# Kernel optimization log

Hardware: AMD Instinct MI355X
Metric: run time of the kernel (lower is better)

The kernel has to match this reference:

```python
import jax, jax.numpy as jnp
import numpy as np

D_MODEL = 1024
NUM_HEADS = 16
SEG = 512            # segment_size
DIL = 4              # dilation_rate
HEAD_DIM = D_MODEL // NUM_HEADS


def setup_inputs() -> dict:
    key = jax.random.key(0)
    ks = jax.random.split(key, 5)
    B, S = 4, 4096
    sc = D_MODEL ** -0.5  # keep projected activations O(1) so softmax is not saturated
    def w(k):
        return jax.random.normal(k, (D_MODEL, D_MODEL), jnp.float32) * sc
    z = jnp.zeros((D_MODEL,), jnp.float32)
    return {
        "x": jax.random.normal(ks[0], (B, S, D_MODEL), jnp.float32),
        "Wq": w(ks[1]), "bq": z,
        "Wk": w(ks[2]), "bk": z,
        "Wv": w(ks[3]), "bv": z,
        "Wo": w(ks[4]), "bo": z,
    }


def reference(x, Wq, bq, Wk, bk, Wv, bv, Wo, bo):
    B, S, D = x.shape
    H, hd, seg, r = NUM_HEADS, HEAD_DIM, SEG, DIL
    scaling = hd ** -0.5

    Q = x @ Wq + bq
    K = x @ Wk + bk
    V = x @ Wv + bv

    pad = (-S) % seg
    if pad:
        Q = jnp.pad(Q, ((0, 0), (0, pad), (0, 0)))
        K = jnp.pad(K, ((0, 0), (0, pad), (0, 0)))
        V = jnp.pad(V, ((0, 0), (0, pad), (0, 0)))
    n = (S + pad) // seg          # num_segments
    sd = seg // r                 # dilated positions per segment per head

    # [B, n, sd, r, H, hd]: position within segment = t*r + offset
    def split(t):
        return t.reshape(B, n, sd, r, H, hd)

    offs = jnp.arange(H) % r      # per-head dilation offset sj = j % r
    hidx = jnp.arange(H)
    # vectorized per-head dilated gather -> [B, n, sd, H, hd]
    Qs = split(Q)[:, :, :, offs, hidx, :]
    Ks = split(K)[:, :, :, offs, hidx, :]
    Vs = split(V)[:, :, :, offs, hidx, :]

    # diagonal q.k score per dilated position, softmax over the segment's dilated positions
    scores = jnp.einsum('bnshd,bnshd->bnsh', Qs, Ks) * scaling
    probs = jax.nn.softmax(scores, axis=2)
    attn = probs[..., None] * Vs  # [B, n, sd, H, hd]

    # scatter back to each head's dilated positions; other positions stay zero
    out = jnp.zeros((B, n, sd, r, H, hd), x.dtype)
    out = out.at[:, :, :, offs, hidx, :].set(attn)
    out = out.reshape(B, n * seg, D)[:, :S]
    return out @ Wo + bo
```

## Files before the change

kernel.cpp:

```cpp
#include <hip/hip_runtime.h>
#include <hip/hip_bf16.h>

typedef unsigned short u16;
typedef unsigned int u32;
typedef __attribute__((ext_vector_type(8))) __bf16 bf16x8;
typedef __attribute__((ext_vector_type(4))) float f32x4;

#define NB 4
#define SQ 4096
#define DM 1024
#define RPC 4096
#define S4 (4 * DM)

#define VMCNT(n) asm volatile("s_waitcnt vmcnt(" #n ")" ::: "memory")
#define BARRIER() asm volatile("s_barrier" ::: "memory")

__device__ __forceinline__ u16 f2b(float f) {
  u32 u = __builtin_bit_cast(u32, f);
  u32 r = u + 0x7fffu + ((u >> 16) & 1u);
  return (u16)(r >> 16);
}
__device__ __forceinline__ u32 cvt2(float lo, float hi) {
  u16 a = __builtin_bit_cast(u16, __float2bfloat16(lo));
  u16 b = __builtin_bit_cast(u16, __float2bfloat16(hi));
  return (u32)a | ((u32)b << 16);
}
__device__ __forceinline__ float dot2(u32 q, u32 k) {
  float ql = __builtin_bit_cast(float, q << 16);
  float qh = __builtin_bit_cast(float, q & 0xffff0000u);
  float kl = __builtin_bit_cast(float, k << 16);
  float kh = __builtin_bit_cast(float, k & 0xffff0000u);
  return ql * kl + qh * kh;
}
__device__ __forceinline__ u32 mul2(u32 v, float p) {
  float lo = __builtin_bit_cast(float, v << 16) * p;
  float hi = __builtin_bit_cast(float, v & 0xffff0000u) * p;
  return (u32)f2b(lo) | ((u32)f2b(hi) << 16);
}
__device__ __forceinline__ void gll16(const void* g, void* l) {
  __builtin_amdgcn_global_load_lds(
      (const __attribute__((address_space(1))) void*)g,
      (__attribute__((address_space(3))) void*)l, 16, 0, 0);
}

__global__ __launch_bounds__(256) void pack_x(const float* __restrict__ x,
                                              u16* __restrict__ xbT) {
  const int tid = threadIdx.x;
  const int wv = tid >> 6, l = tid & 63;
  const int gr0 = blockIdx.x * 16 + wv * 4;
#pragma unroll
  for (int it = 0; it < 4; ++it) {
    const int gr = gr0 + it;
    const int c = gr >> 12, pr = gr & 4095;
    const int b = pr >> 10;
    const int srow = ((pr & 1023) << 2) + c;
    const int m0 = pr >> 8, rloc = pr & 255;
    const float* src = x + ((size_t)(b * SQ) + srow) * DM;
    u16* dimg = xbT + (size_t)((c * 16 + m0) * 16) * 16384 + rloc * 64;
    const int swzbase = ((((l & 15) >> 1) ^ (rloc & 7)) << 3) + (l & 1) * 4;
#pragma unroll
    for (int i = 0; i < 4; ++i) {
      float4 v = *reinterpret_cast<const float4*>(src + i * 256 + l * 4);
      uint2 pk;
      pk.x = cvt2(v.x, v.y);
      pk.y = cvt2(v.z, v.w);
      const int k64 = i * 4 + (l >> 4);
      *reinterpret_cast<uint2*>(dimg + (size_t)k64 * 16384 + swzbase) = pk;
    }
  }
}

__global__ __launch_bounds__(256) void trans_qkv(const float* __restrict__ Wq,
                                                 const float* __restrict__ Wk,
                                                 const float* __restrict__ Wv,
                                                 u16* __restrict__ WTp) {
  __shared__ float T[64][65];
  const int k0 = blockIdx.x * 64, j0 = blockIdx.y * 64, c = blockIdx.z;
  const int msel = j0 >> 8;
  const float* W = (msel == 0) ? Wq : ((msel == 1) ? Wk : Wv);
  const int slot = (j0 & 255) >> 6;
  const int colbase = (c + 4 * slot) * 64;
  const int tid = threadIdx.x;
  const int rr = tid >> 6, cc = tid & 63;
#pragma unroll
  for (int it = 0; it < 16; ++it) {
    const int kk = rr + it * 4;
    T[kk][cc] = W[(size_t)(k0 + kk) * 1024 + colbase + cc];
  }
  __syncthreads();
  const int k64 = k0 >> 6;
  const int u = cc >> 3, e = cc & 7;
#pragma unroll
  for (int it = 0; it < 16; ++it) {
    const int jj = rr + it * 4;
    const int j = j0 + jj;
    const int n0 = j / 192, nrow = j - n0 * 192;
    WTp[((size_t)((c * 4 + n0) * 16 + k64)) * 12288 + nrow * 64 + (((u ^ (nrow & 7))) << 3) + e] =
        f2b(T[cc][jj]);
  }
}

__global__ __launch_bounds__(256) void trans_wo(const float* __restrict__ Wo,
                                                u16* __restrict__ WoTp) {
  __shared__ float T[64][65];
  const int j0 = blockIdx.x * 64, e0 = blockIdx.y * 64, c = blockIdx.z;
  const int rowbase = c * 64 + (j0 >> 6) * 256;
  const int tid = threadIdx.x;
  const int rr = tid >> 6, cc = tid & 63;
#pragma unroll
  for (int it = 0; it < 16; ++it) {
    const int jj = rr + it * 4;
    T[jj][cc] = Wo[(size_t)(rowbase + jj) * 1024 + e0 + cc];
  }
  __syncthreads();
  const int k64 = j0 >> 6;
  const int u = cc >> 3, e = cc & 7;
#pragma unroll
  for (int it = 0; it < 16; ++it) {
    const int ee = rr + it * 4;
    const int n = e0 + ee;
    const int n0 = n >> 8, nrow = n & 255;
    WoTp[((size_t)((c * 4 + n0) * 4 + k64)) * 16384 + nrow * 64 + (((u ^ (nrow & 7))) << 3) + e] =
        f2b(T[cc][ee]);
  }
}

__global__ __launch_bounds__(256) void bias_pack(const float* __restrict__ bq,
                                                 const float* __restrict__ bk,
                                                 const float* __restrict__ bv,
                                                 float* __restrict__ biasp) {
  const int idx = blockIdx.x * 256 + threadIdx.x;
  if (idx >= 3072) return;
  const int c = idx / 768, j = idx % 768;
  const int msel = j >> 8, jj = j & 255;
  const int col = (c + 4 * (jj >> 6)) * 64 + (jj & 63);
  const float* bb = (msel == 0) ? bq : ((msel == 1) ? bk : bv);
  biasp[idx] = bb[col];
}

__global__ __launch_bounds__(512, 1) void gemm_qkv(const u16* __restrict__ xbT,
                                                   const u16* __restrict__ WTp,
                                                   const float* __restrict__ biasp,
                                                   u16* __restrict__ QKV) {
  __shared__ __align__(16) u16 As3[3 * 16384];
  __shared__ __align__(16) u16 Bs2[2 * 12288];
  const int p = blockIdx.x;
  const int L = (p & 7) * 32 + (p >> 3);
  const int c = L >> 6, rem = L & 63;
  const int m0 = rem >> 2, n0 = rem & 3;
  const int tid = threadIdx.x;
  const int lane = tid & 63, w = tid >> 6;
  const int wm = w >> 1, wn = w & 1;
  const int l15 = lane & 15, l16 = lane >> 4;

  const u16* Asrc = xbT + (size_t)((c * 16 + m0) * 16) * 16384;
  const u16* Bsrc = WTp + (size_t)((c * 4 + n0) * 16) * 12288;

  f32x4 acc[4][6];
#pragma unroll
  for (int i = 0; i < 4; ++i)
#pragma unroll
    for (int j = 0; j < 6; ++j) acc[i][j] = (f32x4){0.f, 0.f, 0.f, 0.f};

  int abase[2], bbase[2];
#pragma unroll
  for (int kk = 0; kk < 2; ++kk) {
    const int unit = kk * 4 + l16;
    abase[kk] = (wm * 64 + l15) * 64 + ((unit ^ (l15 & 7)) << 3);
    bbase[kk] = (wn * 96 + l15) * 64 + ((unit ^ (l15 & 7)) << 3);
  }

#define ISSUE_A(kt, buf)                                                   \
  {                                                                        \
    _Pragma("unroll") for (int i = 0; i < 4; ++i)                          \
        gll16(Asrc + (size_t)(kt) * 16384 + tid * 8 + i * 4096,            \
              (char*)As3 + (buf) * 32768 + tid * 16 + i * 8192);           \
  }
#define ISSUE_B(kt, buf)                                                   \
  {                                                                        \
    _Pragma("unroll") for (int i = 0; i < 3; ++i)                          \
        gll16(Bsrc + (size_t)(kt) * 12288 + tid * 8 + i * 4096,            \
              (char*)Bs2 + (buf) * 24576 + tid * 16 + i * 8192);           \
  }

  ISSUE_A(0, 0);
  ISSUE_B(0, 0);
  ISSUE_A(1, 1);
  ISSUE_B(1, 1);
  ISSUE_A(2, 2);
  VMCNT(11);
  BARRIER();

  int abuf = 0, bbuf = 0;
#pragma unroll 1
  for (int t = 0; t < 16; ++t) {
    const u16* Ab = As3 + abuf * 16384;
    const u16* Bb = Bs2 + bbuf * 12288;
#pragma unroll
    for (int kk = 0; kk < 2; ++kk) {
      bf16x8 af[4], bv[6];
#pragma unroll
      for (int mf = 0; mf < 4; ++mf)
        af[mf] = *reinterpret_cast<const bf16x8*>(Ab + abase[kk] + mf * 1024);
#pragma unroll
      for (int nf = 0; nf < 6; ++nf)
        bv[nf] = *reinterpret_cast<const bf16x8*>(Bb + bbase[kk] + nf * 1024);
      __builtin_amdgcn_s_setprio(1);
#pragma unroll
      for (int mf = 0; mf < 4; ++mf)
#pragma unroll
        for (int nf = 0; nf < 6; ++nf)
          acc[mf][nf] = __builtin_amdgcn_mfma_f32_16x16x32_bf16(af[mf], bv[nf], acc[mf][nf], 0, 0, 0);
      __builtin_amdgcn_s_setprio(0);
    }
    if (t == 15) break;
    BARRIER();
    if (t <= 12) ISSUE_A(t + 3, abuf);
    if (t <= 13) ISSUE_B(t + 2, bbuf);
    if (t <= 12) { VMCNT(7); }
    else if (t == 13) { VMCNT(3); }
    else { VMCNT(0); }
    BARRIER();
    abuf = (abuf == 2) ? 0 : abuf + 1;
    bbuf ^= 1;
  }
#undef ISSUE_A
#undef ISSUE_B

  const int rbase = m0 * 256;
  u16* outc = QKV + (size_t)c * RPC * 768;
#pragma unroll
  for (int mf = 0; mf < 4; ++mf) {
#pragma unroll
    for (int nf = 0; nf < 6; ++nf) {
      const int gcol = n0 * 192 + wn * 96 + nf * 16 + l15;
      const float bias = biasp[c * 768 + gcol];
#pragma unroll
      for (int jj = 0; jj < 4; ++jj) {
        const int rowt = wm * 64 + mf * 16 + l16 * 4 + jj;
        outc[(size_t)(rbase + rowt) * 768 + gcol] = f2b(acc[mf][nf][jj] + bias);
      }
    }
  }
}

__global__ __launch_bounds__(256) void attn_k(const u16* __restrict__ QKV,
                                              u16* __restrict__ attnYp) {
  __shared__ float sc[4][128];
  const int blk = blockIdx.x;
  const int c = blk >> 6, b = (blk >> 4) & 3, n = (blk >> 1) & 7, half = blk & 1;
  const int r0 = b * 1024 + n * 128;
  const int m0 = r0 >> 8;
  const int rb = r0 & 255;
  const u16* base = QKV + ((size_t)c * RPC + r0) * 768;
  const int tid = threadIdx.x;
#pragma unroll
  for (int it = 0; it < 2; ++it) {
    const int tt = tid + it * 256;
    const int t = tt & 127, slot = tt >> 7;
    const u16* q = base + (size_t)t * 768 + slot * 64;
    float s = 0.f;
#pragma unroll
    for (int dd = 0; dd < 8; ++dd) {
      uint4 qa = *reinterpret_cast<const uint4*>(q + dd * 8);
      uint4 ka = *reinterpret_cast<const uint4*>(q + 256 + dd * 8);
      s += dot2(qa.x, ka.x) + dot2(qa.y, ka.y) + dot2(qa.z, ka.z) + dot2(qa.w, ka.w);
    }
    sc[slot][t] = s * 0.125f;
  }
  __syncthreads();
  const int w = tid >> 6, lane = tid & 63;
  float v0 = sc[w][lane], v1 = sc[w][lane + 64];
  float m = fmaxf(v0, v1);
#pragma unroll
  for (int off = 32; off; off >>= 1) m = fmaxf(m, __shfl_xor(m, off));
  float e0 = __expf(v0 - m), e1 = __expf(v1 - m);
  float ssum = e0 + e1;
#pragma unroll
  for (int off = 32; off; off >>= 1) ssum += __shfl_xor(ssum, off);
  const float inv = 1.f / ssum;
  sc[w][lane] = e0 * inv;
  sc[w][lane + 64] = e1 * inv;
  __syncthreads();
  u16* yout = attnYp + (size_t)((c * 16 + m0) * 4) * 16384;
#pragma unroll
  for (int it = 0; it < 8; ++it) {
    const int vi = tid + it * 256;
    const int t = vi >> 4, c8 = (vi & 15) + half * 16;
    const float pr = sc[c8 >> 3][t];
    uint4 va = *reinterpret_cast<const uint4*>(base + (size_t)t * 768 + 512 + c8 * 8);
    uint4 ra;
    ra.x = mul2(va.x, pr); ra.y = mul2(va.y, pr); ra.z = mul2(va.z, pr); ra.w = mul2(va.w, pr);
    const int rloc = rb + t;
    const int k64 = c8 >> 3, uu = c8 & 7, pp = uu ^ (rloc & 7);
    *reinterpret_cast<uint4*>(yout + k64 * 16384 + rloc * 64 + pp * 8) = ra;
  }
}

__global__ __launch_bounds__(512, 1) void gemm_out(const u16* __restrict__ attnYp,
                                                   const u16* __restrict__ WoTp,
                                                   const float* __restrict__ bo,
                                                   float* __restrict__ out) {
  __shared__ __align__(16) u16 As[2][16384];
  __shared__ __align__(16) u16 Bs[2][16384];
  const int p = blockIdx.x;
  const int L = (p & 7) * 32 + (p >> 3);
  const int c = L >> 6, rem = L & 63;
  const int m0 = rem >> 2, n0 = rem & 3;
  const int tid = threadIdx.x;
  const int lane = tid & 63, w = tid >> 6;
  const int wm = w >> 1, wn = w & 1;
  const int l15 = lane & 15, l16 = lane >> 4;

  const u16* Asrc = attnYp + (size_t)((c * 16 + m0) * 4) * 16384;
  const u16* Bsrc = WoTp + (size_t)((c * 4 + n0) * 4) * 16384;

  f32x4 acc[4][8];
#pragma unroll
  for (int i = 0; i < 4; ++i)
#pragma unroll
    for (int j = 0; j < 8; ++j) acc[i][j] = (f32x4){0.f, 0.f, 0.f, 0.f};

  int aoff[2][4], boff[2][8];
#pragma unroll
  for (int kk = 0; kk < 2; ++kk) {
    const int unit = kk * 4 + l16;
#pragma unroll
    for (int mf = 0; mf < 4; ++mf) {
      const int r = wm * 64 + mf * 16 + l15;
      aoff[kk][mf] = r * 64 + ((unit ^ (r & 7)) << 3);
    }
#pragma unroll
    for (int nf = 0; nf < 8; ++nf) {
      const int r = wn * 128 + nf * 16 + l15;
      boff[kk][nf] = r * 64 + ((unit ^ (r & 7)) << 3);
    }
  }

#define ISSUE(kt, buf)                                                     \
  {                                                                        \
    _Pragma("unroll") for (int i = 0; i < 4; ++i) {                        \
      gll16(Asrc + (size_t)(kt) * 16384 + tid * 8 + i * 4096,              \
            (char*)&As[buf][0] + tid * 16 + i * 8192);                     \
      gll16(Bsrc + (size_t)(kt) * 16384 + tid * 8 + i * 4096,              \
            (char*)&Bs[buf][0] + tid * 16 + i * 8192);                     \
    }                                                                      \
  }

  ISSUE(0, 0);
  ISSUE(1, 1);
  VMCNT(8);
  BARRIER();

#pragma unroll 1
  for (int t = 0; t < 4; ++t) {
    const u16* Ab = As[t & 1];
    const u16* Bb = Bs[t & 1];
#pragma unroll
    for (int kk = 0; kk < 2; ++kk) {
      bf16x8 af[4], bv[8];
#pragma unroll
      for (int mf = 0; mf < 4; ++mf) af[mf] = *reinterpret_cast<const bf16x8*>(Ab + aoff[kk][mf]);
#pragma unroll
      for (int nf = 0; nf < 8; ++nf) bv[nf] = *reinterpret_cast<const bf16x8*>(Bb + boff[kk][nf]);
      __builtin_amdgcn_s_setprio(1);
#pragma unroll
      for (int mf = 0; mf < 4; ++mf)
#pragma unroll
        for (int nf = 0; nf < 8; ++nf)
          acc[mf][nf] = __builtin_amdgcn_mfma_f32_16x16x32_bf16(af[mf], bv[nf], acc[mf][nf], 0, 0, 0);
      __builtin_amdgcn_s_setprio(0);
    }
    if (t == 3) break;
    BARRIER();
    if (t <= 1) {
      ISSUE(t + 2, t & 1);
      VMCNT(8);
    } else {
      VMCNT(0);
    }
    BARRIER();
  }
#undef ISSUE

  const int rbase = m0 * 256;
  const int b = rbase >> 10;
  const int sbase = ((rbase & 1023) << 2) + c;
  float* outp = out + (size_t)(b * SQ + sbase) * DM;
#pragma unroll
  for (int mf = 0; mf < 4; ++mf) {
#pragma unroll
    for (int nf = 0; nf < 8; ++nf) {
      const int gcol = n0 * 256 + wn * 128 + nf * 16 + l15;
      const float bias = bo[gcol];
#pragma unroll
      for (int jj = 0; jj < 4; ++jj) {
        const int rowt = wm * 64 + mf * 16 + l16 * 4 + jj;
        outp[(size_t)rowt * S4 + gcol] = acc[mf][nf][jj] + bias;
      }
    }
  }
}

extern "C" void kernel_launch(void* const* d_in, const int* in_sizes, int n_in,
                              void* d_out, int out_size, void* d_ws, size_t ws_size,
                              hipStream_t stream) {
  const float* x  = (const float*)d_in[0];
  const float* Wq = (const float*)d_in[1];
  const float* bq = (const float*)d_in[2];
  const float* Wk = (const float*)d_in[3];
  const float* bk = (const float*)d_in[4];
  const float* Wv = (const float*)d_in[5];
  const float* bv = (const float*)d_in[6];
  const float* Wo = (const float*)d_in[7];
  const float* bo = (const float*)d_in[8];
  float* out = (float*)d_out;

  char* ws = (char*)d_ws;
  u16* xbT    = (u16*)(ws);
  u16* WoTp   = (u16*)(ws + 33554432);
  u16* attnYp = (u16*)(ws + 35651584);

  char* ob = (char*)d_out;
  u16*   QKV   = (u16*)(ob);
  u16*   WTp   = (u16*)(ob + 33554432);
  float* biasp = (float*)(ob + 39845888);

  pack_x<<<1024, 256, 0, stream>>>(x, xbT);
  trans_qkv<<<dim3(16, 12, 4), 256, 0, stream>>>(Wq, Wk, Wv, WTp);
  bias_pack<<<12, 256, 0, stream>>>(bq, bk, bv, biasp);
  trans_wo<<<dim3(4, 16, 4), 256, 0, stream>>>(Wo, WoTp);
  gemm_qkv<<<256, 512, 0, stream>>>(xbT, WTp, biasp, QKV);
  attn_k<<<256, 256, 0, stream>>>(QKV, attnYp);
  gemm_out<<<256, 512, 0, stream>>>(attnYp, WoTp, bo, out);
}
```

Baseline: 98.01 us.

## Fuse prep kernels into one launch and halve QKV GEMM M-tile for two blocks per CU

The four preprocessing kernels (x pack, QKV weight transpose, Wo transpose, bias pack) are merged into a single kernel that dispatches on block index, saving launch overhead and gaps between kernels. The QKV GEMM moves from 512-thread blocks with a 256-row tile and triple-buffered A to 256-thread blocks with a 128-row tile and double buffering. That doubles the grid to 512 and allows two blocks per CU. The cost is more redundant B-tile loads per output and a shallower prefetch pipeline.

```diff
diff --git a/kernel.cpp b/kernel.cpp
--- a/kernel.cpp
+++ b/kernel.cpp
@@ -43,117 +43,123 @@
       (__attribute__((address_space(3))) void*)l, 16, 0, 0);
 }
 
-__global__ __launch_bounds__(256) void pack_x(const float* __restrict__ x,
-                                              u16* __restrict__ xbT) {
+__global__ __launch_bounds__(256) void prep(const float* __restrict__ x,
+                                            const float* __restrict__ Wq,
+                                            const float* __restrict__ Wk,
+                                            const float* __restrict__ Wv,
+                                            const float* __restrict__ Wo,
+                                            const float* __restrict__ bq,
+                                            const float* __restrict__ bk,
+                                            const float* __restrict__ bv,
+                                            u16* __restrict__ xbT,
+                                            u16* __restrict__ WTp,
+                                            u16* __restrict__ WoTp,
+                                            float* __restrict__ biasp) {
+  __shared__ float T[64][65];
+  const int bid = blockIdx.x;
   const int tid = threadIdx.x;
-  const int wv = tid >> 6, l = tid & 63;
-  const int gr0 = blockIdx.x * 16 + wv * 4;
-#pragma unroll
-  for (int it = 0; it < 4; ++it) {
-    const int gr = gr0 + it;
-    const int c = gr >> 12, pr = gr & 4095;
-    const int b = pr >> 10;
-    const int srow = ((pr & 1023) << 2) + c;
-    const int m0 = pr >> 8, rloc = pr & 255;
-    const float* src = x + ((size_t)(b * SQ) + srow) * DM;
-    u16* dimg = xbT + (size_t)((c * 16 + m0) * 16) * 16384 + rloc * 64;
-    const int swzbase = ((((l & 15) >> 1) ^ (rloc & 7)) << 3) + (l & 1) * 4;
-#pragma unroll
-    for (int i = 0; i < 4; ++i) {
-      float4 v = *reinterpret_cast<const float4*>(src + i * 256 + l * 4);
-      uint2 pk;
-      pk.x = cvt2(v.x, v.y);
-      pk.y = cvt2(v.z, v.w);
-      const int k64 = i * 4 + (l >> 4);
-      *reinterpret_cast<uint2*>(dimg + (size_t)k64 * 16384 + swzbase) = pk;
-    }
-  }
-}
-
-__global__ __launch_bounds__(256) void trans_qkv(const float* __restrict__ Wq,
-                                                 const float* __restrict__ Wk,
-                                                 const float* __restrict__ Wv,
-                                                 u16* __restrict__ WTp) {
-  __shared__ float T[64][65];
-  const int k0 = blockIdx.x * 64, j0 = blockIdx.y * 64, c = blockIdx.z;
-  const int msel = j0 >> 8;
-  const float* W = (msel == 0) ? Wq : ((msel == 1) ? Wk : Wv);
-  const int slot = (j0 & 255) >> 6;
-  const int colbase = (c + 4 * slot) * 64;
-  const int tid = threadIdx.x;
-  const int rr = tid >> 6, cc = tid & 63;
-#pragma unroll
-  for (int it = 0; it < 16; ++it) {
-    const int kk = rr + it * 4;
-    T[kk][cc] = W[(size_t)(k0 + kk) * 1024 + colbase + cc];
-  }
-  __syncthreads();
-  const int k64 = k0 >> 6;
-  const int u = cc >> 3, e = cc & 7;
-#pragma unroll
-  for (int it = 0; it < 16; ++it) {
-    const int jj = rr + it * 4;
-    const int j = j0 + jj;
-    const int n0 = j / 192, nrow = j - n0 * 192;
-    WTp[((size_t)((c * 4 + n0) * 16 + k64)) * 12288 + nrow * 64 + (((u ^ (nrow & 7))) << 3) + e] =
-        f2b(T[cc][jj]);
-  }
-}
-
-__global__ __launch_bounds__(256) void trans_wo(const float* __restrict__ Wo,
-                                                u16* __restrict__ WoTp) {
-  __shared__ float T[64][65];
-  const int j0 = blockIdx.x * 64, e0 = blockIdx.y * 64, c = blockIdx.z;
-  const int rowbase = c * 64 + (j0 >> 6) * 256;
-  const int tid = threadIdx.x;
-  const int rr = tid >> 6, cc = tid & 63;
-#pragma unroll
-  for (int it = 0; it < 16; ++it) {
-    const int jj = rr + it * 4;
-    T[jj][cc] = Wo[(size_t)(rowbase + jj) * 1024 + e0 + cc];
-  }
-  __syncthreads();
-  const int k64 = j0 >> 6;
-  const int u = cc >> 3, e = cc & 7;
-#pragma unroll
-  for (int it = 0; it < 16; ++it) {
-    const int ee = rr + it * 4;
-    const int n = e0 + ee;
-    const int n0 = n >> 8, nrow = n & 255;
-    WoTp[((size_t)((c * 4 + n0) * 4 + k64)) * 16384 + nrow * 64 + (((u ^ (nrow & 7))) << 3) + e] =
-        f2b(T[cc][ee]);
-  }
-}
-
-__global__ __launch_bounds__(256) void bias_pack(const float* __restrict__ bq,
-                                                 const float* __restrict__ bk,
-                                                 const float* __restrict__ bv,
-                                                 float* __restrict__ biasp) {
-  const int idx = blockIdx.x * 256 + threadIdx.x;
-  if (idx >= 3072) return;
-  const int c = idx / 768, j = idx % 768;
-  const int msel = j >> 8, jj = j & 255;
-  const int col = (c + 4 * (jj >> 6)) * 64 + (jj & 63);
-  const float* bb = (msel == 0) ? bq : ((msel == 1) ? bk : bv);
-  biasp[idx] = bb[col];
-}
-
-__global__ __launch_bounds__(512, 1) void gemm_qkv(const u16* __restrict__ xbT,
+  if (bid < 1024) {
+    const int wv = tid >> 6, l = tid & 63;
+    const int gr0 = bid * 16 + wv * 4;
+#pragma unroll
+    for (int it = 0; it < 4; ++it) {
+      const int gr = gr0 + it;
+      const int c = gr >> 12, pr = gr & 4095;
+      const int b = pr >> 10;
+      const int srow = ((pr & 1023) << 2) + c;
+      const int m0 = pr >> 8, rloc = pr & 255;
+      const float* src = x + ((size_t)(b * SQ) + srow) * DM;
+      u16* dimg = xbT + (size_t)((c * 16 + m0) * 16) * 16384 + rloc * 64;
+      const int swzbase = ((((l & 15) >> 1) ^ (rloc & 7)) << 3) + (l & 1) * 4;
+#pragma unroll
+      for (int i = 0; i < 4; ++i) {
+        float4 v = *reinterpret_cast<const float4*>(src + i * 256 + l * 4);
+        uint2 pk;
+        pk.x = cvt2(v.x, v.y);
+        pk.y = cvt2(v.z, v.w);
+        const int k64 = i * 4 + (l >> 4);
+        *reinterpret_cast<uint2*>(dimg + (size_t)k64 * 16384 + swzbase) = pk;
+      }
+    }
+  } else if (bid < 1792) {
+    const int q = bid - 1024;
+    const int c = q / 192;
+    const int rem = q - c * 192;
+    const int j0 = (rem >> 4) * 64;
+    const int k0 = (rem & 15) * 64;
+    const int msel = j0 >> 8;
+    const float* W = (msel == 0) ? Wq : ((msel == 1) ? Wk : Wv);
+    const int slot = (j0 & 255) >> 6;
+    const int colbase = (c + 4 * slot) * 64;
+    const int rr = tid >> 6, cc = tid & 63;
+#pragma unroll
+    for (int it = 0; it < 16; ++it) {
+      const int kk = rr + it * 4;
+      T[kk][cc] = W[(size_t)(k0 + kk) * 1024 + colbase + cc];
+    }
+    __syncthreads();
+    const int k64 = k0 >> 6;
+    const int u = cc >> 3, e = cc & 7;
+#pragma unroll
+    for (int it = 0; it < 16; ++it) {
+      const int jj = rr + it * 4;
+      const int j = j0 + jj;
+      const int n0 = j / 192, nrow = j - n0 * 192;
+      WTp[((size_t)((c * 4 + n0) * 16 + k64)) * 12288 + nrow * 64 + (((u ^ (nrow & 7))) << 3) + e] =
+          f2b(T[cc][jj]);
+    }
+  } else if (bid < 2048) {
+    const int q = bid - 1792;
+    const int c = q >> 6;
+    const int rem = q & 63;
+    const int e0 = (rem >> 2) * 64;
+    const int j0 = (rem & 3) * 64;
+    const int rowbase = c * 64 + (j0 >> 6) * 256;
+    const int rr = tid >> 6, cc = tid & 63;
+#pragma unroll
+    for (int it = 0; it < 16; ++it) {
+      const int jj = rr + it * 4;
+      T[jj][cc] = Wo[(size_t)(rowbase + jj) * 1024 + e0 + cc];
+    }
+    __syncthreads();
+    const int k64 = j0 >> 6;
+    const int u = cc >> 3, e = cc & 7;
+#pragma unroll
+    for (int it = 0; it < 16; ++it) {
+      const int ee = rr + it * 4;
+      const int n = e0 + ee;
+      const int n0 = n >> 8, nrow = n & 255;
+      WoTp[((size_t)((c * 4 + n0) * 4 + k64)) * 16384 + nrow * 64 + (((u ^ (nrow & 7))) << 3) + e] =
+          f2b(T[cc][ee]);
+    }
+  } else {
+    const int idx = (bid - 2048) * 256 + tid;
+    if (idx < 3072) {
+      const int c = idx / 768, j = idx % 768;
+      const int msel = j >> 8, jj = j & 255;
+      const int col = (c + 4 * (jj >> 6)) * 64 + (jj & 63);
+      const float* bb = (msel == 0) ? bq : ((msel == 1) ? bk : bv);
+      biasp[idx] = bb[col];
+    }
+  }
+}
+
+__global__ __launch_bounds__(256, 2) void gemm_qkv(const u16* __restrict__ xbT,
                                                    const u16* __restrict__ WTp,
                                                    const float* __restrict__ biasp,
                                                    u16* __restrict__ QKV) {
-  __shared__ __align__(16) u16 As3[3 * 16384];
+  __shared__ __align__(16) u16 As2[2 * 8192];
   __shared__ __align__(16) u16 Bs2[2 * 12288];
   const int p = blockIdx.x;
-  const int L = (p & 7) * 32 + (p >> 3);
-  const int c = L >> 6, rem = L & 63;
-  const int m0 = rem >> 2, n0 = rem & 3;
+  const int L = (p & 7) * 64 + (p >> 3);
+  const int c = L >> 7, r = L & 127;
+  const int m0 = r >> 2, n0 = r & 3;
   const int tid = threadIdx.x;
   const int lane = tid & 63, w = tid >> 6;
   const int wm = w >> 1, wn = w & 1;
   const int l15 = lane & 15, l16 = lane >> 4;
 
-  const u16* Asrc = xbT + (size_t)((c * 16 + m0) * 16) * 16384;
+  const u16* Asrc = xbT + (size_t)((c * 16 + (m0 >> 1)) * 16) * 16384 + (m0 & 1) * 8192;
   const u16* Bsrc = WTp + (size_t)((c * 4 + n0) * 16) * 12288;
 
   f32x4 acc[4][6];
@@ -173,29 +179,27 @@
 #define ISSUE_A(kt, buf)                                                   \
   {                                                                        \
     _Pragma("unroll") for (int i = 0; i < 4; ++i)                          \
-        gll16(Asrc + (size_t)(kt) * 16384 + tid * 8 + i * 4096,            \
-              (char*)As3 + (buf) * 32768 + tid * 16 + i * 8192);           \
+        gll16(Asrc + (size_t)(kt) * 16384 + i * 2048 + tid * 8,            \
+              (char*)As2 + (buf) * 16384 + i * 4096 + tid * 16);           \
   }
 #define ISSUE_B(kt, buf)                                                   \
   {                                                                        \
-    _Pragma("unroll") for (int i = 0; i < 3; ++i)                          \
-        gll16(Bsrc + (size_t)(kt) * 12288 + tid * 8 + i * 4096,            \
-              (char*)Bs2 + (buf) * 24576 + tid * 16 + i * 8192);           \
+    _Pragma("unroll") for (int i = 0; i < 6; ++i)                          \
+        gll16(Bsrc + (size_t)(kt) * 12288 + i * 2048 + tid * 8,            \
+              (char*)Bs2 + (buf) * 24576 + i * 4096 + tid * 16);           \
   }
 
   ISSUE_A(0, 0);
   ISSUE_B(0, 0);
   ISSUE_A(1, 1);
   ISSUE_B(1, 1);
-  ISSUE_A(2, 2);
-  VMCNT(11);
+  VMCNT(10);
   BARRIER();
 
-  int abuf = 0, bbuf = 0;
 #pragma unroll 1
   for (int t = 0; t < 16; ++t) {
-    const u16* Ab = As3 + abuf * 16384;
-    const u16* Bb = Bs2 + bbuf * 12288;
+    const u16* Ab = As2 + (t & 1) * 8192;
+    const u16* Bb = Bs2 + (t & 1) * 12288;
 #pragma unroll
     for (int kk = 0; kk < 2; ++kk) {
       bf16x8 af[4], bv[6];
@@ -215,19 +219,19 @@
     }
     if (t == 15) break;
     BARRIER();
-    if (t <= 12) ISSUE_A(t + 3, abuf);
-    if (t <= 13) ISSUE_B(t + 2, bbuf);
-    if (t <= 12) { VMCNT(7); }
-    else if (t == 13) { VMCNT(3); }
-    else { VMCNT(0); }
+    if (t <= 13) {
+      ISSUE_A(t + 2, t & 1);
+      ISSUE_B(t + 2, t & 1);
+      VMCNT(10);
+    } else {
+      VMCNT(0);
+    }
     BARRIER();
-    abuf = (abuf == 2) ? 0 : abuf + 1;
-    bbuf ^= 1;
   }
 #undef ISSUE_A
 #undef ISSUE_B
 
-  const int rbase = m0 * 256;
+  const int rbase = m0 * 128;
   u16* outc = QKV + (size_t)c * RPC * 768;
 #pragma unroll
   for (int mf = 0; mf < 4; ++mf) {
@@ -426,11 +430,8 @@
   u16*   WTp   = (u16*)(ob + 33554432);
   float* biasp = (float*)(ob + 39845888);
 
-  pack_x<<<1024, 256, 0, stream>>>(x, xbT);
-  trans_qkv<<<dim3(16, 12, 4), 256, 0, stream>>>(Wq, Wk, Wv, WTp);
-  bias_pack<<<12, 256, 0, stream>>>(bq, bk, bv, biasp);
-  trans_wo<<<dim3(4, 16, 4), 256, 0, stream>>>(Wo, WoTp);
-  gemm_qkv<<<256, 512, 0, stream>>>(xbT, WTp, biasp, QKV);
+  prep<<<2060, 256, 0, stream>>>(x, Wq, Wk, Wv, Wo, bq, bk, bv, xbT, WTp, WoTp, biasp);
+  gemm_qkv<<<512, 256, 0, stream>>>(xbT, WTp, biasp, QKV);
   attn_k<<<256, 256, 0, stream>>>(QKV, attnYp);
   gemm_out<<<256, 512, 0, stream>>>(attnYp, WoTp, bo, out);
 }
```

Result: faster. 88.33 us (-9.9%).
